# Performance work log

Measured on AMD Instinct MI355X. Metric: run time of the kernel, lower is better.

Reference implementation:

```python
import jax, jax.numpy as jnp
import numpy as np

TOL = 1e-4
MAX_ITER = 50
D = 512
B = 16384

def setup_inputs() -> dict:
    key = jax.random.key(0)
    kx, kw = jax.random.split(key)
    x = jax.random.normal(kx, (B, D), dtype=jnp.float32)
    # nn.Linear default init: U(-1/sqrt(d), 1/sqrt(d)), bias=False
    bound = 1.0 / np.sqrt(D)
    W = jax.random.uniform(kw, (D, D), dtype=jnp.float32, minval=-bound, maxval=bound)
    return {"x": x, "W": W}

def reference(x, W):
    # Fixed-point iteration z <- tanh(z @ W^T + x).
    # Torch uses a data-dependent while loop with early break; here we run a
    # fixed-length scan and freeze z once the convergence criterion fires,
    # which reproduces the same converged value (z is held constant after
    # ||z_next - z|| < tol, exactly like breaking out of the loop).
    z0 = jnp.zeros_like(x)

    def step(carry, _):
        z, done = carry
        z_next = jnp.tanh(z @ W.T + x)          # [B, D]
        err = jnp.linalg.norm(z_next - z)        # global Frobenius norm, like torch.norm
        z_new = jnp.where(done, z, z_next)       # freeze after convergence (early-exit)
        done = done | (err < TOL)
        return (z_new, done), None

    (z, _), _ = jax.lax.scan(step, (z0, jnp.array(False)), None, length=MAX_ITER)
    return z
```

## Files before the change

### kernel.cpp

```cpp
#include <hip/hip_runtime.h>


typedef short s8v  __attribute__((ext_vector_type(8)));
typedef float f32x16 __attribute__((ext_vector_type(16)));

#define BATCH 16384
#define DIM   512
#define TM    64
#define NITER 50

__device__ __forceinline__ unsigned short f2bf(float f) {
    unsigned int u = __float_as_uint(f);
    u += 0x7fffu + ((u >> 16) & 1u);
    return (unsigned short)(u >> 16);
}

__device__ __forceinline__ float fast_tanh(float v) {
    v = fminf(10.0f, fmaxf(-10.0f, v));
    float t = __builtin_amdgcn_exp2f(v * 2.8853900817779268f);
    return (t - 1.0f) * __builtin_amdgcn_rcpf(t + 1.0f);
}

__device__ __forceinline__ f32x16 zero16() {
    f32x16 v;
#pragma unroll
    for (int i = 0; i < 16; ++i) v[i] = 0.0f;
    return v;
}

__global__ void wprep_kernel(const float* __restrict__ W, unsigned short* __restrict__ Wf) {
    int tid = blockIdx.x * blockDim.x + threadIdx.x;
    int jt  = tid >> 11;
    int rem = tid & 2047;
    int ks  = rem >> 6;
    int L   = rem & 63;
    int j   = jt * 32 + (L & 31);
    int k   = ks * 16 + (L >> 5) * 8;
    const float* src = W + j * DIM + k;
    uint4 p;
    p.x = (unsigned)f2bf(src[0]) | ((unsigned)f2bf(src[1]) << 16);
    p.y = (unsigned)f2bf(src[2]) | ((unsigned)f2bf(src[3]) << 16);
    p.z = (unsigned)f2bf(src[4]) | ((unsigned)f2bf(src[5]) << 16);
    p.w = (unsigned)f2bf(src[6]) | ((unsigned)f2bf(src[7]) << 16);
    ((uint4*)Wf)[tid] = p;
}

__device__ __forceinline__ int z_addr(int r, int j) {
    int c  = j >> 3;
    int lo = j & 7;
    return r * DIM + (((c ^ (r & 7)) << 3) | lo);
}

__global__ __launch_bounds__(512, 2)
void fixpoint_kernel(const float* __restrict__ x,
                     const unsigned short* __restrict__ Wf,
                     float* __restrict__ out) {
    __shared__ alignas(16) unsigned short zt[TM * DIM];

    const int tid  = threadIdx.x;
    const int lane = tid & 63;
    const int w    = tid >> 6;
    const int l31  = lane & 31;
    const int h    = lane >> 5;
    const int r0   = blockIdx.x * TM;
    const int jt0  = 2 * w;

    for (int idx = tid; idx < TM * DIM; idx += 512) {
        int r = idx >> 9, j = idx & (DIM - 1);
        zt[z_addr(r, j)] = f2bf(fast_tanh(x[(size_t)(r0 + r) * DIM + j]));
    }
    __syncthreads();

    const s8v* Wfv = (const s8v*)Wf;
    const int swz = l31 & 7;

    for (int it = 0; it < NITER - 1; ++it) {
        f32x16 acc00 = zero16(), acc01 = zero16(), acc10 = zero16(), acc11 = zero16();

#pragma unroll 4
        for (int ks = 0; ks < 32; ++ks) {
            s8v a0 = Wfv[(jt0 * 32 + ks) * 64 + lane];
            s8v a1 = Wfv[((jt0 + 1) * 32 + ks) * 64 + lane];
            int c = ((2 * ks + h) ^ swz) << 3;
            s8v b0 = *(const s8v*)&zt[l31 * DIM + c];
            s8v b1 = *(const s8v*)&zt[(l31 + 32) * DIM + c];
            acc00 = __builtin_amdgcn_mfma_f32_32x32x16_bf16(a0, b0, acc00, 0, 0, 0);
            acc01 = __builtin_amdgcn_mfma_f32_32x32x16_bf16(a0, b1, acc01, 0, 0, 0);
            acc10 = __builtin_amdgcn_mfma_f32_32x32x16_bf16(a1, b0, acc10, 0, 0, 0);
            acc11 = __builtin_amdgcn_mfma_f32_32x32x16_bf16(a1, b1, acc11, 0, 0, 0);
        }
        __syncthreads();

        const bool last = (it == NITER - 2);

        auto epi = [&](const f32x16& acc, int jb, int rl) {
            const size_t rowoff = (size_t)(r0 + rl) * DIM;
#pragma unroll
            for (int g = 0; g < 4; ++g) {
                int j0 = jb + 8 * g + 4 * h;
                const float4 xv = *(const float4*)&x[rowoff + j0];
                float v0 = fast_tanh(acc[4 * g + 0] + xv.x);
                float v1 = fast_tanh(acc[4 * g + 1] + xv.y);
                float v2 = fast_tanh(acc[4 * g + 2] + xv.z);
                float v3 = fast_tanh(acc[4 * g + 3] + xv.w);
                uint2 p;
                p.x = (unsigned)f2bf(v0) | ((unsigned)f2bf(v1) << 16);
                p.y = (unsigned)f2bf(v2) | ((unsigned)f2bf(v3) << 16);
                *(uint2*)&zt[z_addr(rl, j0)] = p;
                if (last) {
                    float4 o; o.x = v0; o.y = v1; o.z = v2; o.w = v3;
                    *(float4*)&out[rowoff + j0] = o;
                }
            }
        };
        epi(acc00, w * 64,      l31);
        epi(acc01, w * 64,      l31 + 32);
        epi(acc10, w * 64 + 32, l31);
        epi(acc11, w * 64 + 32, l31 + 32);
        __syncthreads();
    }
}

extern "C" void kernel_launch(void* const* d_in, const int* in_sizes, int n_in,
                              void* d_out, int out_size, void* d_ws, size_t ws_size,
                              hipStream_t stream) {
    const float* x = (const float*)d_in[0];
    const float* W = (const float*)d_in[1];
    float* out = (float*)d_out;
    unsigned short* Wf = (unsigned short*)d_ws;

    wprep_kernel<<<128, 256, 0, stream>>>(W, Wf);
    fixpoint_kernel<<<BATCH / TM, 512, 0, stream>>>(x, Wf, out);
}
```

Before: 609.5 us.

## Double-buffer z in LDS, keep x in registers as MFMA accumulator init

Result: slower. 1.243 ms (+103.9%).

```diff
diff --git a/kernel.cpp b/kernel.cpp
--- a/kernel.cpp
+++ b/kernel.cpp
@@ -13,19 +13,6 @@
     unsigned int u = __float_as_uint(f);
     u += 0x7fffu + ((u >> 16) & 1u);
     return (unsigned short)(u >> 16);
-}
-
-__device__ __forceinline__ float fast_tanh(float v) {
-    v = fminf(10.0f, fmaxf(-10.0f, v));
-    float t = __builtin_amdgcn_exp2f(v * 2.8853900817779268f);
-    return (t - 1.0f) * __builtin_amdgcn_rcpf(t + 1.0f);
-}
-
-__device__ __forceinline__ f32x16 zero16() {
-    f32x16 v;
-#pragma unroll
-    for (int i = 0; i < 16; ++i) v[i] = 0.0f;
-    return v;
 }
 
 __global__ void wprep_kernel(const float* __restrict__ W, unsigned short* __restrict__ Wf) {
@@ -51,11 +38,26 @@
     return r * DIM + (((c ^ (r & 7)) << 3) | lo);
 }
 
+__device__ __forceinline__ unsigned pk_bf16(float lo, float hi) {
+    unsigned r;
+    asm("v_cvt_pk_bf16_f32 %0, %1, %2" : "=v"(r) : "v"(lo), "v"(hi));
+    return r;
+}
+
+__device__ __forceinline__ float tanh1(float v) {
+    const float K  = 2.8853900817779268f;
+    const float CL = 28.853900817779268f;
+    float s = __builtin_amdgcn_fmed3f(v * K, -CL, CL);
+    float t = __builtin_amdgcn_exp2f(s);
+    float q = __builtin_amdgcn_rcpf(t + 1.0f);
+    return fmaf(-2.0f, q, 1.0f);
+}
+
 __global__ __launch_bounds__(512, 2)
 void fixpoint_kernel(const float* __restrict__ x,
                      const unsigned short* __restrict__ Wf,
                      float* __restrict__ out) {
-    __shared__ alignas(16) unsigned short zt[TM * DIM];
+    __shared__ alignas(16) unsigned short zt[2][TM * DIM];
 
     const int tid  = threadIdx.x;
     const int lane = tid & 63;
@@ -64,61 +66,121 @@
     const int h    = lane >> 5;
     const int r0   = blockIdx.x * TM;
     const int jt0  = 2 * w;
+    const int jb0  = 64 * w;
+    const int swz  = l31 & 7;
 
-    for (int idx = tid; idx < TM * DIM; idx += 512) {
-        int r = idx >> 9, j = idx & (DIM - 1);
-        zt[z_addr(r, j)] = f2bf(fast_tanh(x[(size_t)(r0 + r) * DIM + j]));
+    const s8v* Wfv = (const s8v*)Wf;
+
+    f32x16 xs0, xs1, xs2, xs3;
+    {
+        const float* xr0 = x + (size_t)(r0 + l31) * DIM;
+        const float* xr1 = x + (size_t)(r0 + l31 + 32) * DIM;
+#pragma unroll
+        for (int g = 0; g < 4; ++g) {
+            const int j0 = jb0 + 8 * g + 4 * h;
+            float4 t0 = *(const float4*)&xr0[j0];
+            float4 t1 = *(const float4*)&xr1[j0];
+            float4 t2 = *(const float4*)&xr0[j0 + 32];
+            float4 t3 = *(const float4*)&xr1[j0 + 32];
+            xs0[4*g+0] = t0.x; xs0[4*g+1] = t0.y; xs0[4*g+2] = t0.z; xs0[4*g+3] = t0.w;
+            xs1[4*g+0] = t1.x; xs1[4*g+1] = t1.y; xs1[4*g+2] = t1.z; xs1[4*g+3] = t1.w;
+            xs2[4*g+0] = t2.x; xs2[4*g+1] = t2.y; xs2[4*g+2] = t2.z; xs2[4*g+3] = t2.w;
+            xs3[4*g+0] = t3.x; xs3[4*g+1] = t3.y; xs3[4*g+2] = t3.z; xs3[4*g+3] = t3.w;
+        }
     }
+
+    const s8v pa0 = Wfv[(jt0 * 32) * 64 + lane];
+    const s8v pa1 = Wfv[((jt0 + 1) * 32) * 64 + lane];
+
+    f32x16 ac0, ac1, ac2, ac3;
+
+    auto epi_z = [&](const f32x16& A0, const f32x16& A1, const f32x16& A2, const f32x16& A3,
+                     unsigned short* __restrict__ zn) {
+#pragma unroll
+        for (int g = 0; g < 4; ++g) {
+            const int j0 = jb0 + 8 * g + 4 * h;
+            {
+                uint2 p;
+                p.x = pk_bf16(tanh1(A0[4*g+0]), tanh1(A0[4*g+1]));
+                p.y = pk_bf16(tanh1(A0[4*g+2]), tanh1(A0[4*g+3]));
+                *(uint2*)&zn[z_addr(l31, j0)] = p;
+            }
+            {
+                uint2 p;
+                p.x = pk_bf16(tanh1(A1[4*g+0]), tanh1(A1[4*g+1]));
+                p.y = pk_bf16(tanh1(A1[4*g+2]), tanh1(A1[4*g+3]));
+                *(uint2*)&zn[z_addr(l31 + 32, j0)] = p;
+            }
+            {
+                uint2 p;
+                p.x = pk_bf16(tanh1(A2[4*g+0]), tanh1(A2[4*g+1]));
+                p.y = pk_bf16(tanh1(A2[4*g+2]), tanh1(A2[4*g+3]));
+                *(uint2*)&zn[z_addr(l31, j0 + 32)] = p;
+            }
+            {
+                uint2 p;
+                p.x = pk_bf16(tanh1(A3[4*g+0]), tanh1(A3[4*g+1]));
+                p.y = pk_bf16(tanh1(A3[4*g+2]), tanh1(A3[4*g+3]));
+                *(uint2*)&zn[z_addr(l31 + 32, j0 + 32)] = p;
+            }
+        }
+    };
+
+    auto epi_out = [&](const f32x16& A0, const f32x16& A1, const f32x16& A2, const f32x16& A3) {
+        float* o0 = out + (size_t)(r0 + l31) * DIM;
+        float* o1 = out + (size_t)(r0 + l31 + 32) * DIM;
+#pragma unroll
+        for (int g = 0; g < 4; ++g) {
+            const int j0 = jb0 + 8 * g + 4 * h;
+            float4 v;
+            v.x = tanh1(A0[4*g+0]); v.y = tanh1(A0[4*g+1]); v.z = tanh1(A0[4*g+2]); v.w = tanh1(A0[4*g+3]);
+            *(float4*)&o0[j0] = v;
+            v.x = tanh1(A1[4*g+0]); v.y = tanh1(A1[4*g+1]); v.z = tanh1(A1[4*g+2]); v.w = tanh1(A1[4*g+3]);
+            *(float4*)&o1[j0] = v;
+            v.x = tanh1(A2[4*g+0]); v.y = tanh1(A2[4*g+1]); v.z = tanh1(A2[4*g+2]); v.w = tanh1(A2[4*g+3]);
+            *(float4*)&o0[j0 + 32] = v;
+            v.x = tanh1(A3[4*g+0]); v.y = tanh1(A3[4*g+1]); v.z = tanh1(A3[4*g+2]); v.w = tanh1(A3[4*g+3]);
+            *(float4*)&o1[j0 + 32] = v;
+        }
+    };
+
+    auto gemm = [&](const unsigned short* __restrict__ zc) {
+        {
+            const int c0 = (h ^ swz) << 3;
+            s8v b0 = *(const s8v*)&zc[l31 * DIM + c0];
+            s8v b1 = *(const s8v*)&zc[(l31 + 32) * DIM + c0];
+            ac0 = __builtin_amdgcn_mfma_f32_32x32x16_bf16(pa0, b0, xs0, 0, 0, 0);
+            ac1 = __builtin_amdgcn_mfma_f32_32x32x16_bf16(pa0, b1, xs1, 0, 0, 0);
+            ac2 = __builtin_amdgcn_mfma_f32_32x32x16_bf16(pa1, b0, xs2, 0, 0, 0);
+            ac3 = __builtin_amdgcn_mfma_f32_32x32x16_bf16(pa1, b1, xs3, 0, 0, 0);
+        }
+#pragma unroll 4
+        for (int ks = 1; ks < 32; ++ks) {
+            s8v a0 = Wfv[(jt0 * 32 + ks) * 64 + lane];
+            s8v a1 = Wfv[((jt0 + 1) * 32 + ks) * 64 + lane];
+            const int c = ((2 * ks + h) ^ swz) << 3;
+            s8v b0 = *(const s8v*)&zc[l31 * DIM + c];
+            s8v b1 = *(const s8v*)&zc[(l31 + 32) * DIM + c];
+            ac0 = __builtin_amdgcn_mfma_f32_32x32x16_bf16(a0, b0, ac0, 0, 0, 0);
+            ac1 = __builtin_amdgcn_mfma_f32_32x32x16_bf16(a0, b1, ac1, 0, 0, 0);
+            ac2 = __builtin_amdgcn_mfma_f32_32x32x16_bf16(a1, b0, ac2, 0, 0, 0);
+            ac3 = __builtin_amdgcn_mfma_f32_32x32x16_bf16(a1, b1, ac3, 0, 0, 0);
+        }
+    };
+
+    epi_z(xs0, xs1, xs2, xs3, zt[0]);
     __syncthreads();
 
-    const s8v* Wfv = (const s8v*)Wf;
-    const int swz = l31 & 7;
-
-    for (int it = 0; it < NITER - 1; ++it) {
-        f32x16 acc00 = zero16(), acc01 = zero16(), acc10 = zero16(), acc11 = zero16();
-
-#pragma unroll 4
-        for (int ks = 0; ks < 32; ++ks) {
-            s8v a0 = Wfv[(jt0 * 32 + ks) * 64 + lane];
-            s8v a1 = Wfv[((jt0 + 1) * 32 + ks) * 64 + lane];
-            int c = ((2 * ks + h) ^ swz) << 3;
-            s8v b0 = *(const s8v*)&zt[l31 * DIM + c];
-            s8v b1 = *(const s8v*)&zt[(l31 + 32) * DIM + c];
-            acc00 = __builtin_amdgcn_mfma_f32_32x32x16_bf16(a0, b0, acc00, 0, 0, 0);
-            acc01 = __builtin_amdgcn_mfma_f32_32x32x16_bf16(a0, b1, acc01, 0, 0, 0);
-            acc10 = __builtin_amdgcn_mfma_f32_32x32x16_bf16(a1, b0, acc10, 0, 0, 0);
-            acc11 = __builtin_amdgcn_mfma_f32_32x32x16_bf16(a1, b1, acc11, 0, 0, 0);
-        }
+    int cur = 0;
+#pragma unroll 1
+    for (int it = 0; it < NITER - 2; ++it) {
+        gemm(zt[cur]);
+        epi_z(ac0, ac1, ac2, ac3, zt[cur ^ 1]);
         __syncthreads();
-
-        const bool last = (it == NITER - 2);
-
-        auto epi = [&](const f32x16& acc, int jb, int rl) {
-            const size_t rowoff = (size_t)(r0 + rl) * DIM;
-#pragma unroll
-            for (int g = 0; g < 4; ++g) {
-                int j0 = jb + 8 * g + 4 * h;
-                const float4 xv = *(const float4*)&x[rowoff + j0];
-                float v0 = fast_tanh(acc[4 * g + 0] + xv.x);
-                float v1 = fast_tanh(acc[4 * g + 1] + xv.y);
-                float v2 = fast_tanh(acc[4 * g + 2] + xv.z);
-                float v3 = fast_tanh(acc[4 * g + 3] + xv.w);
-                uint2 p;
-                p.x = (unsigned)f2bf(v0) | ((unsigned)f2bf(v1) << 16);
-                p.y = (unsigned)f2bf(v2) | ((unsigned)f2bf(v3) << 16);
-                *(uint2*)&zt[z_addr(rl, j0)] = p;
-                if (last) {
-                    float4 o; o.x = v0; o.y = v1; o.z = v2; o.w = v3;
-                    *(float4*)&out[rowoff + j0] = o;
-                }
-            }
-        };
-        epi(acc00, w * 64,      l31);
-        epi(acc01, w * 64,      l31 + 32);
-        epi(acc10, w * 64 + 32, l31);
-        epi(acc11, w * 64 + 32, l31 + 32);
-        __syncthreads();
+        cur ^= 1;
     }
+    gemm(zt[cur]);
+    epi_out(ac0, ac1, ac2, ac3);
 }
 
 extern "C" void kernel_launch(void* const* d_in, const int* in_sizes, int n_in,
```
